# Kernel tuning notes

Hardware: AMD Instinct MI355X
Metric: run time of the kernel (lower is better)

The kernel has to match this reference:

```python
import jax, jax.numpy as jnp
import numpy as np

B, C, T = 128, 9, 2048
R = T // 4            # reduced_timesteps after two MaxPool1d(2)
N = B * R             # total graph nodes
E_SINGLE = 8192       # edges per sample graph (avg degree 16 over R nodes)
HID = 128
OUT = 12


def setup_inputs():
    key = jax.random.key(0)
    ks = jax.random.split(key, 14)
    x = jax.random.normal(ks[0], (B, C, T), jnp.float32)
    # per-sample graph, replicated with offset i*R per batch element (as in forward)
    single = jax.random.randint(ks[1], (2, E_SINGLE), 0, R)
    offsets = (jnp.arange(B) * R)[None, :, None]
    edge_index = (single[:, None, :] + offsets).reshape(2, -1)  # [2, B*E_SINGLE]

    def lin(k, fan_in, shape):
        return jax.random.normal(k, shape, jnp.float32) / np.sqrt(fan_in)

    return {
        "x": x,
        "edge_index": edge_index,
        "conv1_w": lin(ks[2], C * 5, (16, C, 5)),
        "conv1_b": jnp.zeros((16,), jnp.float32),
        "conv2_w": lin(ks[3], 16 * 5, (32, 16, 5)),
        "conv2_b": jnp.zeros((32,), jnp.float32),
        "gcn1_w": lin(ks[4], 32, (32, HID)),
        "gcn1_b": jnp.zeros((HID,), jnp.float32),
        "gcn2_w": lin(ks[5], HID, (HID, HID)),
        "gcn2_b": jnp.zeros((HID,), jnp.float32),
        "fc_w": lin(ks[6], HID, (HID, OUT)),
        "fc_b": jnp.zeros((OUT,), jnp.float32),
    }


def _gcn_conv(h, edge_index, w, b, n):
    # PyG GCNConv: linear -> add self-loops -> sym-normalized sum aggregation -> + bias
    h = h @ w
    loops = jnp.arange(n)
    row = jnp.concatenate([edge_index[0], loops])  # source
    col = jnp.concatenate([edge_index[1], loops])  # target (aggregation)
    deg = jax.ops.segment_sum(jnp.ones(col.shape, h.dtype), col, num_segments=n)
    dis = jnp.where(deg > 0, jax.lax.rsqrt(jnp.maximum(deg, 1e-12)), 0.0)
    norm = dis[row] * dis[col]                      # [E+N]
    out = jax.ops.segment_sum(norm[:, None] * h[row], col, num_segments=n)
    return out + b


def _temporal_conv(x, w1, b1, w2, b2):
    dn = ("NCH", "OIH", "NCH")
    h = jax.lax.conv_general_dilated(x, w1, (1,), [(2, 2)], dimension_numbers=dn)
    h = jax.nn.relu(h + b1[None, :, None])
    h = jax.lax.reduce_window(h, -jnp.inf, jax.lax.max, (1, 1, 2), (1, 1, 2), "VALID")
    h = jax.lax.conv_general_dilated(h, w2, (1,), [(2, 2)], dimension_numbers=dn)
    h = jax.nn.relu(h + b2[None, :, None])
    h = jax.lax.reduce_window(h, -jnp.inf, jax.lax.max, (1, 1, 2), (1, 1, 2), "VALID")
    return h  # [B, 32, R]


def reference(x, edge_index, conv1_w, conv1_b, conv2_w, conv2_b,
              gcn1_w, gcn1_b, gcn2_w, gcn2_b, fc_w, fc_b):
    h = _temporal_conv(x, conv1_w, conv1_b, conv2_w, conv2_b)   # [B, 32, R]
    nodes = h.transpose(0, 2, 1).reshape(B * R, 32)             # [N, 32]
    g = jax.nn.relu(_gcn_conv(nodes, edge_index, gcn1_w, gcn1_b, N))
    g = jax.nn.relu(_gcn_conv(g, edge_index, gcn2_w, gcn2_b, N))
    g = g.reshape(B, R, HID).mean(axis=1)                       # [B, HID]
    return g @ fc_w + fc_b                                      # [B, OUT]
```

## Files before the change

### kernel.cpp

```cpp
#include <hip/hip_runtime.h>
#include <hip/hip_bf16.h>

#define BB   128
#define CIN  9
#define TT   2048
#define RR   512
#define NN   (BB*RR)
#define HID  128
#define NOUT 12

typedef __attribute__((ext_vector_type(8))) short short8;
typedef __attribute__((ext_vector_type(4))) float f32x4;

static __device__ inline unsigned short f2bf(float f) {
    unsigned int u = __float_as_uint(f);
    unsigned int r = (u + 0x7fffu + ((u >> 16) & 1u)) >> 16;
    return (unsigned short)r;
}
static __device__ inline float bf2f(unsigned short u) {
    return __uint_as_float(((unsigned int)u) << 16);
}

__global__ __launch_bounds__(512) void k_convs(const float* __restrict__ x,
        const float* __restrict__ w1, const float* __restrict__ b1,
        const float* __restrict__ w2, const float* __restrict__ b2,
        unsigned short* __restrict__ nodesT,
        const int* __restrict__ ei, int E, int es,
        unsigned short* __restrict__ Ab16,
        const float* __restrict__ g2w, unsigned short* __restrict__ w2t,
        float* __restrict__ meanbuf, int* __restrict__ done) {
    __shared__ __align__(16) union {
        struct { float sx[CIN][268]; float s1[16][132]; } c;
        struct { int cnt[512]; float arow[8][512]; } a;
    } u;
    int tid = threadIdx.x;
    int bid = blockIdx.x;

    if (bid == 0) {
        float4 z = make_float4(0.f, 0.f, 0.f, 0.f);
        for (int i = tid; i < 128 * 128 / 4; i += 512) ((float4*)meanbuf)[i] = z;
        if (tid < 128) done[tid] = 0;
        for (int idx = tid; idx < 128 * 128; idx += 512) {
            int c2 = idx >> 7, f = idx & 127;
            w2t[f * 128 + c2] = f2bf(g2w[idx]);
        }
        return;
    }

    if (bid <= 64) {
        int base = (bid - 1) * 8;
        u.a.cnt[tid] = 0;
        float4 z = make_float4(0.f, 0.f, 0.f, 0.f);
        float4* az = (float4*)u.a.arow;
        az[tid] = z; az[tid + 512] = z;
        __syncthreads();
        for (int i = tid; i < es; i += 512) atomicAdd(&u.a.cnt[ei[E + i]], 1);
        __syncthreads();
        for (int i = tid; i < es; i += 512) {
            int c = ei[E + i];
            if (c >= base && c < base + 8) {
                int r = ei[i];
                float nd = rsqrtf((float)u.a.cnt[r] + 1.0f);
                float dn = rsqrtf((float)u.a.cnt[c] + 1.0f);
                atomicAdd(&u.a.arow[c - base][r], nd * dn);
            }
        }
        if (tid < 8) {
            int r = base + tid;
            float d = rsqrtf((float)u.a.cnt[r] + 1.0f);
            atomicAdd(&u.a.arow[tid][r], d * d);
        }
        __syncthreads();
        {
            int row = tid >> 6, c0 = (tid & 63) * 8;
            const float* p = &u.a.arow[row][c0];
            ushort4 o0, o1;
            o0.x = f2bf(p[0]); o0.y = f2bf(p[1]); o0.z = f2bf(p[2]); o0.w = f2bf(p[3]);
            o1.x = f2bf(p[4]); o1.y = f2bf(p[5]); o1.z = f2bf(p[6]); o1.w = f2bf(p[7]);
            *(ushort4*)&Ab16[(size_t)(base + row) * 512 + c0]     = o0;
            *(ushort4*)&Ab16[(size_t)(base + row) * 512 + c0 + 4] = o1;
        }
        return;
    }

    int cb = bid - 65;
    int b  = cb >> 3;
    int r0 = (cb & 7) * 64;
    int wv   = __builtin_amdgcn_readfirstlane(tid >> 6);
    int lane = tid & 63;

    for (int idx = tid; idx < CIN * 268; idx += 512) {
        int c = idx / 268, j = idx - c * 268;
        int g = 4 * r0 - 6 + j;
        float v = 0.f;
        if (g >= 0 && g < TT) v = x[(b * CIN + c) * TT + g];
        u.c.sx[c][j] = v;
    }
    __syncthreads();

    {
        int c1a = wv * 2, c1b = wv * 2 + 1;
        float biasA = b1[c1a], biasB = b1[c1b];
        for (int pp = lane; pp < 132; pp += 64) {
            int p = 2 * r0 - 2 + pp;
            float valA = 0.f, valB = 0.f;
            if (p >= 0 && p < 1024) {
                float a0A = biasA, a1A = biasA, a0B = biasB, a1B = biasB;
#pragma unroll
                for (int c = 0; c < CIN; ++c) {
                    const float2* px = (const float2*)&u.c.sx[c][2 * pp];
                    float2 q0 = px[0], q1 = px[1], q2 = px[2];
                    {
                        const float* wp = &w1[(c1a * CIN + c) * 5];
                        float k0 = wp[0], k1 = wp[1], k2 = wp[2], k3 = wp[3], k4 = wp[4];
                        a0A += q0.x*k0 + q0.y*k1 + q1.x*k2 + q1.y*k3 + q2.x*k4;
                        a1A += q0.y*k0 + q1.x*k1 + q1.y*k2 + q2.x*k3 + q2.y*k4;
                    }
                    {
                        const float* wp = &w1[(c1b * CIN + c) * 5];
                        float k0 = wp[0], k1 = wp[1], k2 = wp[2], k3 = wp[3], k4 = wp[4];
                        a0B += q0.x*k0 + q0.y*k1 + q1.x*k2 + q1.y*k3 + q2.x*k4;
                        a1B += q0.y*k0 + q1.x*k1 + q1.y*k2 + q2.x*k3 + q2.y*k4;
                    }
                }
                valA = fmaxf(fmaxf(a0A, a1A), 0.f);
                valB = fmaxf(fmaxf(a0B, a1B), 0.f);
            }
            u.c.s1[c1a][pp] = valA;
            u.c.s1[c1b][pp] = valB;
        }
    }
    __syncthreads();

    int rl = lane;
    float acc0[4], acc1[4];
#pragma unroll
    for (int o = 0; o < 4; ++o) {
        float bv = b2[wv * 4 + o];
        acc0[o] = bv; acc1[o] = bv;
    }
#pragma unroll
    for (int c = 0; c < 16; ++c) {
        const float2* ps = (const float2*)&u.c.s1[c][2 * rl];
        float2 q0 = ps[0], q1 = ps[1], q2 = ps[2];
#pragma unroll
        for (int o = 0; o < 4; ++o) {
            const float* wp = &w2[((wv * 4 + o) * 16 + c) * 5];
            float k0 = wp[0], k1 = wp[1], k2 = wp[2], k3 = wp[3], k4 = wp[4];
            acc0[o] += q0.x*k0 + q0.y*k1 + q1.x*k2 + q1.y*k3 + q2.x*k4;
            acc1[o] += q0.y*k0 + q1.x*k1 + q1.y*k2 + q2.x*k3 + q2.y*k4;
        }
    }
    int n = r0 + rl;
    unsigned short* np = nodesT + ((size_t)b * 32 + wv * 4) * 512 + n;
    np[0]    = f2bf(fmaxf(fmaxf(acc0[0], acc1[0]), 0.f));
    np[512]  = f2bf(fmaxf(fmaxf(acc0[1], acc1[1]), 0.f));
    np[1024] = f2bf(fmaxf(fmaxf(acc0[2], acc1[2]), 0.f));
    np[1536] = f2bf(fmaxf(fmaxf(acc0[3], acc1[3]), 0.f));
}

__global__ __launch_bounds__(256) void k_agg1(const unsigned short* __restrict__ Ab,
        const unsigned short* __restrict__ nT, const float* __restrict__ w1,
        const float* __restrict__ b1, unsigned short* __restrict__ h16) {
    __shared__ unsigned short sA[128][72];
    __shared__ unsigned short sN[32][72];
    __shared__ float sAgg[128][33];
    __shared__ float sw1[32 * 128];
    int tid = threadIdx.x;
    int b  = blockIdx.x >> 2;
    int rb = blockIdx.x & 3;
    int r0 = rb * 128;
    const unsigned short* nb = nT + (size_t)b * 32 * 512;

    {
        const float4* src = (const float4*)w1;
        float4* dst = (float4*)sw1;
#pragma unroll
        for (int i = 0; i < 4; ++i) dst[tid + i * 256] = src[tid + i * 256];
    }

    int wv = tid >> 6, lane = tid & 63;
    int l15 = lane & 15, quad = lane >> 4;
    int mB = wv * 32;
    f32x4 acc[2][2];
#pragma unroll
    for (int i = 0; i < 2; ++i)
#pragma unroll
        for (int j = 0; j < 2; ++j) acc[i][j] = (f32x4){0.f, 0.f, 0.f, 0.f};

    for (int kt = 0; kt < 8; ++kt) {
        int k0 = kt * 64;
        __syncthreads();
#pragma unroll
        for (int i = 0; i < 8; ++i) {
            int idx = tid + i * 256;
            int row = idx >> 4, c4 = (idx & 15) * 4;
            *(ushort4*)&sA[row][c4] = *(const ushort4*)&Ab[(size_t)(r0 + row) * 512 + k0 + c4];
        }
#pragma unroll
        for (int i = 0; i < 2; ++i) {
            int idx = tid + i * 256;
            int f = idx >> 4, c4 = (idx & 15) * 4;
            *(ushort4*)&sN[f][c4] = *(const ushort4*)&nb[(size_t)f * 512 + k0 + c4];
        }
        __syncthreads();
#pragma unroll
        for (int ks = 0; ks < 2; ++ks) {
            int kk = ks * 32 + quad * 8;
            short8 av0 = *(const short8*)&sA[mB + l15][kk];
            short8 av1 = *(const short8*)&sA[mB + 16 + l15][kk];
            short8 bv0 = *(const short8*)&sN[l15][kk];
            short8 bv1 = *(const short8*)&sN[16 + l15][kk];
            acc[0][0] = __builtin_amdgcn_mfma_f32_16x16x32_bf16(av0, bv0, acc[0][0], 0, 0, 0);
            acc[0][1] = __builtin_amdgcn_mfma_f32_16x16x32_bf16(av0, bv1, acc[0][1], 0, 0, 0);
            acc[1][0] = __builtin_amdgcn_mfma_f32_16x16x32_bf16(av1, bv0, acc[1][0], 0, 0, 0);
            acc[1][1] = __builtin_amdgcn_mfma_f32_16x16x32_bf16(av1, bv1, acc[1][1], 0, 0, 0);
        }
    }
    __syncthreads();
#pragma unroll
    for (int mi = 0; mi < 2; ++mi)
#pragma unroll
        for (int ni = 0; ni < 2; ++ni)
#pragma unroll
            for (int r = 0; r < 4; ++r)
                sAgg[mB + mi * 16 + quad * 4 + r][ni * 16 + l15] = acc[mi][ni][r];
    __syncthreads();

    int fq = tid & 31;
    int ng = tid >> 5;
    float4 bv = *(const float4*)&b1[fq * 4];
    for (int ch = 0; ch < 4; ++ch) {
        float a[4][4];
#pragma unroll
        for (int j = 0; j < 4; ++j)
#pragma unroll
            for (int q = 0; q < 4; ++q) a[j][q] = 0.f;
#pragma unroll
        for (int c = 0; c < 32; ++c) {
            float4 wvv = *(const float4*)&sw1[c * 128 + fq * 4];
#pragma unroll
            for (int j = 0; j < 4; ++j) {
                float xc = sAgg[ch * 32 + ng * 4 + j][c];
                a[j][0] += xc * wvv.x; a[j][1] += xc * wvv.y;
                a[j][2] += xc * wvv.z; a[j][3] += xc * wvv.w;
            }
        }
#pragma unroll
        for (int j = 0; j < 4; ++j) {
            ushort4 o;
            o.x = f2bf(fmaxf(a[j][0] + bv.x, 0.f));
            o.y = f2bf(fmaxf(a[j][1] + bv.y, 0.f));
            o.z = f2bf(fmaxf(a[j][2] + bv.z, 0.f));
            o.w = f2bf(fmaxf(a[j][3] + bv.w, 0.f));
            *(ushort4*)&h16[(size_t)(b * 512 + r0 + ch * 32 + ng * 4 + j) * 128 + fq * 4] = o;
        }
    }
}

__global__ __launch_bounds__(256) void k_lin2(const unsigned short* __restrict__ g16,
        const unsigned short* __restrict__ w2t, unsigned short* __restrict__ tT) {
    __shared__ __align__(16) unsigned short smem2[64 * 136 + 128 * 136];
    unsigned short (*srow)[136] = (unsigned short (*)[136])smem2;
    unsigned short (*swT)[136]  = (unsigned short (*)[136])&smem2[64 * 136];
    unsigned short (*sOut)[72]  = (unsigned short (*)[72])smem2;
    int tid = threadIdx.x;
    int nbase = blockIdx.x * 64;

    {
        const ushort4* src = (const ushort4*)(g16 + (size_t)nbase * 128);
#pragma unroll
        for (int i = 0; i < 8; ++i) {
            int idx = tid + i * 256;
            int row = idx >> 5, col4 = idx & 31;
            ushort4 v = src[idx];
            *(ushort4*)&srow[row][col4 * 4] = v;
        }
    }
    {
        const ushort4* src = (const ushort4*)w2t;
#pragma unroll
        for (int i = 0; i < 16; ++i) {
            int idx = tid + i * 256;
            int f = idx >> 5, c4 = idx & 31;
            ushort4 v = src[idx];
            *(ushort4*)&swT[f][c4 * 4] = v;
        }
    }
    __syncthreads();

    int wv  = tid >> 6;
    int lane = tid & 63;
    int m0 = wv * 16;
    int l15 = lane & 15;
    int quad = lane >> 4;
    f32x4 acc[8];
#pragma unroll
    for (int nt = 0; nt < 8; ++nt) acc[nt] = (f32x4){0.f, 0.f, 0.f, 0.f};
#pragma unroll
    for (int kc = 0; kc < 4; ++kc) {
        int k0 = kc * 32 + quad * 8;
        short8 a = *(const short8*)&srow[m0 + l15][k0];
#pragma unroll
        for (int nt = 0; nt < 8; ++nt) {
            short8 b = *(const short8*)&swT[nt * 16 + l15][k0];
            acc[nt] = __builtin_amdgcn_mfma_f32_16x16x32_bf16(a, b, acc[nt], 0, 0, 0);
        }
    }
    __syncthreads();

#pragma unroll
    for (int nt = 0; nt < 8; ++nt) {
        ushort4 o;
        o.x = f2bf(acc[nt][0]); o.y = f2bf(acc[nt][1]);
        o.z = f2bf(acc[nt][2]); o.w = f2bf(acc[nt][3]);
        *(ushort4*)&sOut[nt * 16 + l15][m0 + quad * 4] = o;
    }
    __syncthreads();

    int b = nbase >> 9;
    int rl0 = nbase & 511;
#pragma unroll
    for (int i = 0; i < 8; ++i) {
        int idx = tid + i * 256;
        int col = idx >> 4, r4 = (idx & 15) * 4;
        ushort4 v = *(ushort4*)&sOut[col][r4];
        *(ushort4*)&tT[((size_t)(b * 128 + col)) * 512 + rl0 + r4] = v;
    }
}

__global__ __launch_bounds__(256) void k_agg2(const unsigned short* __restrict__ Ab,
        const unsigned short* __restrict__ tT, const float* __restrict__ b2,
        float* __restrict__ meanbuf, int* __restrict__ done,
        const float* __restrict__ fw, const float* __restrict__ fb,
        float* __restrict__ out) {
    __shared__ unsigned short sA[128][72];
    __shared__ unsigned short sB[128][72];
    __shared__ float sred[2][128];
    __shared__ float sm[HID];
    __shared__ int slast;
    int tid = threadIdx.x;
    int b  = blockIdx.x >> 2;
    int rb = blockIdx.x & 3;
    int r0 = rb * 128;
    const unsigned short* tb = tT + (size_t)b * 128 * 512;
    int wv = tid >> 6, lane = tid & 63;
    int l15 = lane & 15, quad = lane >> 4;
    int wr = wv >> 1, wc = wv & 1;
    f32x4 acc[4][4];
#pragma unroll
    for (int i = 0; i < 4; ++i)
#pragma unroll
        for (int j = 0; j < 4; ++j) acc[i][j] = (f32x4){0.f, 0.f, 0.f, 0.f};

    for (int kt = 0; kt < 8; ++kt) {
        int k0 = kt * 64;
        __syncthreads();
#pragma unroll
        for (int i = 0; i < 8; ++i) {
            int idx = tid + i * 256;
            int row = idx >> 4, c4 = (idx & 15) * 4;
            *(ushort4*)&sA[row][c4] = *(const ushort4*)&Ab[(size_t)(r0 + row) * 512 + k0 + c4];
        }
#pragma unroll
        for (int i = 0; i < 8; ++i) {
            int idx = tid + i * 256;
            int row = idx >> 4, c4 = (idx & 15) * 4;
            *(ushort4*)&sB[row][c4] = *(const ushort4*)&tb[(size_t)row * 512 + k0 + c4];
        }
        __syncthreads();
#pragma unroll
        for (int ks = 0; ks < 2; ++ks) {
            int kk = ks * 32 + quad * 8;
            short8 av[4], bfr[4];
#pragma unroll
            for (int mi = 0; mi < 4; ++mi)
                av[mi] = *(const short8*)&sA[wr * 64 + mi * 16 + l15][kk];
#pragma unroll
            for (int ni = 0; ni < 4; ++ni)
                bfr[ni] = *(const short8*)&sB[wc * 64 + ni * 16 + l15][kk];
#pragma unroll
            for (int mi = 0; mi < 4; ++mi)
#pragma unroll
                for (int ni = 0; ni < 4; ++ni)
                    acc[mi][ni] = __builtin_amdgcn_mfma_f32_16x16x32_bf16(av[mi], bfr[ni], acc[mi][ni], 0, 0, 0);
        }
    }

#pragma unroll
    for (int ni = 0; ni < 4; ++ni) {
        int col = wc * 64 + ni * 16 + l15;
        float bc = b2[col];
        float s = 0.f;
#pragma unroll
        for (int mi = 0; mi < 4; ++mi)
#pragma unroll
            for (int r = 0; r < 4; ++r)
                s += fmaxf(acc[mi][ni][r] + bc, 0.f);
        s += __shfl_xor(s, 16);
        s += __shfl_xor(s, 32);
        if (quad == 0) sred[wr][col] = s;
    }
    __syncthreads();
    if (tid < 128)
        atomicAdd(&meanbuf[b * 128 + tid], (sred[0][tid] + sred[1][tid]) * (1.0f / RR));
    __syncthreads();
    if (tid == 0) {
        __threadfence();
        slast = (atomicAdd(&done[b], 1) == 3) ? 1 : 0;
    }
    __syncthreads();
    if (slast) {
        __threadfence();
        if (tid < HID)
            sm[tid] = __hip_atomic_load(&meanbuf[b * 128 + tid],
                                        __ATOMIC_RELAXED, __HIP_MEMORY_SCOPE_AGENT);
        __syncthreads();
        if (tid < NOUT) {
            float s = fb[tid];
#pragma unroll
            for (int c = 0; c < HID; ++c) s += sm[c] * fw[c * NOUT + tid];
            out[b * NOUT + tid] = s;
        }
    }
}

extern "C" void kernel_launch(void* const* d_in, const int* in_sizes, int n_in,
                              void* d_out, int out_size, void* d_ws, size_t ws_size,
                              hipStream_t stream) {
    const float* x   = (const float*)d_in[0];
    const int*   ei  = (const int*)d_in[1];
    const float* c1w = (const float*)d_in[2];
    const float* c1b = (const float*)d_in[3];
    const float* c2w = (const float*)d_in[4];
    const float* c2b = (const float*)d_in[5];
    const float* g1w = (const float*)d_in[6];
    const float* g1b = (const float*)d_in[7];
    const float* g2w = (const float*)d_in[8];
    const float* g2b = (const float*)d_in[9];
    const float* fw  = (const float*)d_in[10];
    const float* fb  = (const float*)d_in[11];
    float* out = (float*)d_out;
    int E  = in_sizes[1] / 2;
    int es = E / BB;

    char* ws = (char*)d_ws;
    unsigned short* nodesT = (unsigned short*)(ws);
    unsigned short* h1     = (unsigned short*)(ws + (4u << 20));
    unsigned short* tT     = (unsigned short*)(ws + (20u << 20));
    unsigned short* Ab16   = (unsigned short*)(ws + (37u << 20));
    float* meanbuf         = (float*)(ws + (37u << 20) + (512u << 10));
    int*   done            = (int*)  (ws + (37u << 20) + (576u << 10));
    unsigned short* w2t    = (unsigned short*)(ws + (37u << 20) + (772u << 10));

    k_convs<<<1089, 512, 0, stream>>>(x, c1w, c1b, c2w, c2b, nodesT,
                                      ei, E, es, Ab16, g2w, w2t, meanbuf, done);

    k_agg1<<<512, 256, 0, stream>>>(Ab16, nodesT, g1w, g1b, h1);

    k_lin2<<<NN / 64, 256, 0, stream>>>(h1, w2t, tT);
    k_agg2<<<512, 256, 0, stream>>>(Ab16, tT, g2b, meanbuf, done, fw, fb, out);
}
```

Measured before the change: 182.0 us.

## Fuse second GCN linear transform into adjacency aggregation kernel via LDS

```diff
diff --git a/kernel.cpp b/kernel.cpp
--- a/kernel.cpp
+++ b/kernel.cpp
@@ -258,139 +258,132 @@
     }
 }
 
-__global__ __launch_bounds__(256) void k_lin2(const unsigned short* __restrict__ g16,
-        const unsigned short* __restrict__ w2t, unsigned short* __restrict__ tT) {
-    __shared__ __align__(16) unsigned short smem2[64 * 136 + 128 * 136];
-    unsigned short (*srow)[136] = (unsigned short (*)[136])smem2;
-    unsigned short (*swT)[136]  = (unsigned short (*)[136])&smem2[64 * 136];
-    unsigned short (*sOut)[72]  = (unsigned short (*)[72])smem2;
-    int tid = threadIdx.x;
-    int nbase = blockIdx.x * 64;
-
-    {
-        const ushort4* src = (const ushort4*)(g16 + (size_t)nbase * 128);
-#pragma unroll
-        for (int i = 0; i < 8; ++i) {
-            int idx = tid + i * 256;
-            int row = idx >> 5, col4 = idx & 31;
-            ushort4 v = src[idx];
-            *(ushort4*)&srow[row][col4 * 4] = v;
-        }
-    }
-    {
-        const ushort4* src = (const ushort4*)w2t;
-#pragma unroll
-        for (int i = 0; i < 16; ++i) {
-            int idx = tid + i * 256;
-            int f = idx >> 5, c4 = idx & 31;
-            ushort4 v = src[idx];
-            *(ushort4*)&swT[f][c4 * 4] = v;
-        }
-    }
-    __syncthreads();
-
-    int wv  = tid >> 6;
-    int lane = tid & 63;
-    int m0 = wv * 16;
-    int l15 = lane & 15;
-    int quad = lane >> 4;
-    f32x4 acc[8];
-#pragma unroll
-    for (int nt = 0; nt < 8; ++nt) acc[nt] = (f32x4){0.f, 0.f, 0.f, 0.f};
-#pragma unroll
-    for (int kc = 0; kc < 4; ++kc) {
-        int k0 = kc * 32 + quad * 8;
-        short8 a = *(const short8*)&srow[m0 + l15][k0];
-#pragma unroll
-        for (int nt = 0; nt < 8; ++nt) {
-            short8 b = *(const short8*)&swT[nt * 16 + l15][k0];
-            acc[nt] = __builtin_amdgcn_mfma_f32_16x16x32_bf16(a, b, acc[nt], 0, 0, 0);
-        }
-    }
-    __syncthreads();
-
-#pragma unroll
-    for (int nt = 0; nt < 8; ++nt) {
-        ushort4 o;
-        o.x = f2bf(acc[nt][0]); o.y = f2bf(acc[nt][1]);
-        o.z = f2bf(acc[nt][2]); o.w = f2bf(acc[nt][3]);
-        *(ushort4*)&sOut[nt * 16 + l15][m0 + quad * 4] = o;
-    }
-    __syncthreads();
-
-    int b = nbase >> 9;
-    int rl0 = nbase & 511;
-#pragma unroll
-    for (int i = 0; i < 8; ++i) {
-        int idx = tid + i * 256;
-        int col = idx >> 4, r4 = (idx & 15) * 4;
-        ushort4 v = *(ushort4*)&sOut[col][r4];
-        *(ushort4*)&tT[((size_t)(b * 128 + col)) * 512 + rl0 + r4] = v;
-    }
-}
-
-__global__ __launch_bounds__(256) void k_agg2(const unsigned short* __restrict__ Ab,
-        const unsigned short* __restrict__ tT, const float* __restrict__ b2,
+__global__ __launch_bounds__(512) void k_fused2(
+        const unsigned short* __restrict__ h1,
+        const unsigned short* __restrict__ w2t,
+        const unsigned short* __restrict__ Ab,
+        const float* __restrict__ b2,
         float* __restrict__ meanbuf, int* __restrict__ done,
         const float* __restrict__ fw, const float* __restrict__ fb,
         float* __restrict__ out) {
-    __shared__ unsigned short sA[128][72];
-    __shared__ unsigned short sB[128][72];
-    __shared__ float sred[2][128];
-    __shared__ float sm[HID];
-    __shared__ int slast;
-    int tid = threadIdx.x;
-    int b  = blockIdx.x >> 2;
-    int rb = blockIdx.x & 3;
-    int r0 = rb * 128;
-    const unsigned short* tb = tT + (size_t)b * 128 * 512;
-    int wv = tid >> 6, lane = tid & 63;
-    int l15 = lane & 15, quad = lane >> 4;
-    int wr = wv >> 1, wc = wv & 1;
+    __shared__ __align__(16) unsigned short smem[81920];
+    char* tL = (char*)smem;
+    char* sS = (char*)smem + 131072;
+
+    int tid  = threadIdx.x;
+    int smp  = blockIdx.x >> 1;
+    int r0   = (blockIdx.x & 1) * 256;
+    int wv   = __builtin_amdgcn_readfirstlane(tid >> 6);
+    int lane = tid & 63;
+    int l15  = lane & 15, quad = lane >> 4;
+    const unsigned short* hb = h1 + (size_t)smp * 512 * 128;
+
+    short8 w2r[4];
+#pragma unroll
+    for (int ks = 0; ks < 4; ++ks)
+        w2r[ks] = *(const short8*)&w2t[(wv * 16 + l15) * 128 + ks * 32 + quad * 8];
+
+    uint4 stg[4];
+#pragma unroll
+    for (int i = 0; i < 4; ++i) {
+        int idx = tid + i * 512;
+        stg[i] = *(const uint4*)&hb[(size_t)(idx >> 4) * 128 + (idx & 15) * 8];
+    }
+    for (int ch = 0; ch < 4; ++ch) {
+#pragma unroll
+        for (int i = 0; i < 4; ++i) {
+            int idx = tid + i * 512;
+            int row = idx >> 4, c16 = idx & 15;
+            *(uint4*)(sS + row * 256 + ((c16 ^ (row & 7)) << 4)) = stg[i];
+        }
+        __syncthreads();
+        if (ch < 3) {
+#pragma unroll
+            for (int i = 0; i < 4; ++i) {
+                int idx = tid + i * 512;
+                stg[i] = *(const uint4*)&hb[(size_t)((ch + 1) * 128 + (idx >> 4)) * 128 + (idx & 15) * 8];
+            }
+        }
+        f32x4 acc1[8];
+#pragma unroll
+        for (int nf = 0; nf < 8; ++nf) acc1[nf] = (f32x4){0.f, 0.f, 0.f, 0.f};
+#pragma unroll
+        for (int ks = 0; ks < 4; ++ks) {
+#pragma unroll
+            for (int nf = 0; nf < 8; ++nf) {
+                int row = nf * 16 + l15;
+                short8 hf = *(const short8*)(sS + row * 256 + (((ks * 4 + quad) ^ (row & 7)) << 4));
+                acc1[nf] = __builtin_amdgcn_mfma_f32_16x16x32_bf16(w2r[ks], hf, acc1[nf], 0, 0, 0);
+            }
+        }
+#pragma unroll
+        for (int nf = 0; nf < 8; ++nf) {
+#pragma unroll
+            for (int r = 0; r < 4; ++r) {
+                int f = wv * 16 + quad * 4 + r;
+                int node = ch * 128 + nf * 16 + l15;
+                *(unsigned short*)(tL + ((f * 1024 + node * 2) ^ ((f & 7) << 4))) = f2bf(acc1[nf][r]);
+            }
+        }
+        __syncthreads();
+    }
+
+    int m_off = (wv >> 1) * 64;
+    int f_off = (wv & 1) * 64;
     f32x4 acc[4][4];
 #pragma unroll
     for (int i = 0; i < 4; ++i)
 #pragma unroll
         for (int j = 0; j < 4; ++j) acc[i][j] = (f32x4){0.f, 0.f, 0.f, 0.f};
 
+#pragma unroll
+    for (int i = 0; i < 4; ++i) {
+        int idx = tid + i * 512;
+        stg[i] = *(const uint4*)&Ab[(size_t)(r0 + (idx >> 3)) * 512 + (idx & 7) * 8];
+    }
     for (int kt = 0; kt < 8; ++kt) {
-        int k0 = kt * 64;
-        __syncthreads();
-#pragma unroll
-        for (int i = 0; i < 8; ++i) {
-            int idx = tid + i * 256;
-            int row = idx >> 4, c4 = (idx & 15) * 4;
-            *(ushort4*)&sA[row][c4] = *(const ushort4*)&Ab[(size_t)(r0 + row) * 512 + k0 + c4];
-        }
-#pragma unroll
-        for (int i = 0; i < 8; ++i) {
-            int idx = tid + i * 256;
-            int row = idx >> 4, c4 = (idx & 15) * 4;
-            *(ushort4*)&sB[row][c4] = *(const ushort4*)&tb[(size_t)row * 512 + k0 + c4];
-        }
-        __syncthreads();
+#pragma unroll
+        for (int i = 0; i < 4; ++i) {
+            int idx = tid + i * 512;
+            int row = idx >> 3, c16 = idx & 7;
+            *(uint4*)(sS + row * 128 + ((c16 ^ (row & 7)) << 4)) = stg[i];
+        }
+        __syncthreads();
+        if (kt < 7) {
+#pragma unroll
+            for (int i = 0; i < 4; ++i) {
+                int idx = tid + i * 512;
+                stg[i] = *(const uint4*)&Ab[(size_t)(r0 + (idx >> 3)) * 512 + (kt + 1) * 64 + (idx & 7) * 8];
+            }
+        }
 #pragma unroll
         for (int ks = 0; ks < 2; ++ks) {
-            int kk = ks * 32 + quad * 8;
-            short8 av[4], bfr[4];
+            short8 af[4], bfr[4];
+#pragma unroll
+            for (int mi = 0; mi < 4; ++mi) {
+                int row = m_off + mi * 16 + l15;
+                af[mi] = *(const short8*)(sS + row * 128 + (((ks * 4 + quad) ^ (row & 7)) << 4));
+            }
+#pragma unroll
+            for (int ni = 0; ni < 4; ++ni) {
+                int f = f_off + ni * 16 + l15;
+                int k = kt * 64 + ks * 32 + quad * 8;
+                bfr[ni] = *(const short8*)(tL + ((f * 1024 + k * 2) ^ ((f & 7) << 4)));
+            }
 #pragma unroll
             for (int mi = 0; mi < 4; ++mi)
-                av[mi] = *(const short8*)&sA[wr * 64 + mi * 16 + l15][kk];
-#pragma unroll
-            for (int ni = 0; ni < 4; ++ni)
-                bfr[ni] = *(const short8*)&sB[wc * 64 + ni * 16 + l15][kk];
-#pragma unroll
-            for (int mi = 0; mi < 4; ++mi)
 #pragma unroll
                 for (int ni = 0; ni < 4; ++ni)
-                    acc[mi][ni] = __builtin_amdgcn_mfma_f32_16x16x32_bf16(av[mi], bfr[ni], acc[mi][ni], 0, 0, 0);
-        }
-    }
-
+                    acc[mi][ni] = __builtin_amdgcn_mfma_f32_16x16x32_bf16(af[mi], bfr[ni], acc[mi][ni], 0, 0, 0);
+        }
+        __syncthreads();
+    }
+
+    float colsum[4];
 #pragma unroll
     for (int ni = 0; ni < 4; ++ni) {
-        int col = wc * 64 + ni * 16 + l15;
-        float bc = b2[col];
+        int f = f_off + ni * 16 + l15;
+        float bc = b2[f];
         float s = 0.f;
 #pragma unroll
         for (int mi = 0; mi < 4; ++mi)
@@ -399,28 +392,39 @@
                 s += fmaxf(acc[mi][ni][r] + bc, 0.f);
         s += __shfl_xor(s, 16);
         s += __shfl_xor(s, 32);
-        if (quad == 0) sred[wr][col] = s;
-    }
-    __syncthreads();
-    if (tid < 128)
-        atomicAdd(&meanbuf[b * 128 + tid], (sred[0][tid] + sred[1][tid]) * (1.0f / RR));
+        colsum[ni] = s;
+    }
+    float* sred = (float*)sS;
+    float* smv  = sred + 512;
+    int*  slastp = (int*)(smv + 128);
+    if (lane < 16) {
+#pragma unroll
+        for (int ni = 0; ni < 4; ++ni) sred[wv * 64 + ni * 16 + lane] = colsum[ni];
+    }
+    __syncthreads();
+    if (tid < 128) {
+        int half = tid >> 6, fl = tid & 63;
+        float s = sred[(half) * 64 + fl] + sred[(half + 2) * 64 + fl]
+                + sred[(half + 4) * 64 + fl] + sred[(half + 6) * 64 + fl];
+        atomicAdd(&meanbuf[smp * 128 + tid], s * (1.0f / RR));
+    }
     __syncthreads();
     if (tid == 0) {
         __threadfence();
-        slast = (atomicAdd(&done[b], 1) == 3) ? 1 : 0;
-    }
-    __syncthreads();
-    if (slast) {
+        *slastp = (atomicAdd(&done[smp], 1) == 1) ? 1 : 0;
+    }
+    __syncthreads();
+    if (*slastp) {
         __threadfence();
         if (tid < HID)
-            sm[tid] = __hip_atomic_load(&meanbuf[b * 128 + tid],
-                                        __ATOMIC_RELAXED, __HIP_MEMORY_SCOPE_AGENT);
+            smv[tid] = __hip_atomic_load(&meanbuf[smp * 128 + tid],
+                                         __ATOMIC_RELAXED, __HIP_MEMORY_SCOPE_AGENT);
         __syncthreads();
         if (tid < NOUT) {
             float s = fb[tid];
 #pragma unroll
-            for (int c = 0; c < HID; ++c) s += sm[c] * fw[c * NOUT + tid];
-            out[b * NOUT + tid] = s;
+            for (int c = 0; c < HID; ++c) s += smv[c] * fw[c * NOUT + tid];
+            out[smp * NOUT + tid] = s;
         }
     }
 }
@@ -447,7 +451,6 @@
     char* ws = (char*)d_ws;
     unsigned short* nodesT = (unsigned short*)(ws);
     unsigned short* h1     = (unsigned short*)(ws + (4u << 20));
-    unsigned short* tT     = (unsigned short*)(ws + (20u << 20));
     unsigned short* Ab16   = (unsigned short*)(ws + (37u << 20));
     float* meanbuf         = (float*)(ws + (37u << 20) + (512u << 10));
     int*   done            = (int*)  (ws + (37u << 20) + (576u << 10));
@@ -458,6 +461,6 @@
 
     k_agg1<<<512, 256, 0, stream>>>(Ab16, nodesT, g1w, g1b, h1);
 
-    k_lin2<<<NN / 64, 256, 0, stream>>>(h1, w2t, tT);
-    k_agg2<<<512, 256, 0, stream>>>(Ab16, tT, g2b, meanbuf, done, fw, fb, out);
-}
+    k_fused2<<<BB * 2, 512, 0, stream>>>(h1, w2t, Ab16, g2b,
+                                         meanbuf, done, fw, fb, out);
+}
```

After: 200.5 us. 1.1x slower.
